# Performance work log

Measured on AMD Instinct MI355X. Metric: run time of the kernel, lower is better.

Reference implementation:

```python
import jax, jax.numpy as jnp
import numpy as np

N = 100000
E = 1600000
BN_EPS = 1e-5
L2_EPS = 1e-12


def _sage_conv(x, src, dst, wl, bl, wr):
    # mean-aggregate source features onto destination nodes
    s = jax.ops.segment_sum(x[src], dst, num_segments=N)          # [N, C]
    cnt = jax.ops.segment_sum(jnp.ones((E,), x.dtype), dst, num_segments=N)
    agg = s / jnp.maximum(cnt, 1.0)[:, None]
    out = agg @ wl.T + bl + x @ wr.T                              # lin_l(agg) + lin_r(x)
    # normalize=True -> row-wise L2 normalization
    nrm = jnp.sqrt(jnp.sum(out * out, axis=-1, keepdims=True))
    return out / jnp.maximum(nrm, L2_EPS)


def _bn(x, g, b):
    # BatchNorm1d, training-mode batch statistics (biased variance)
    m = jnp.mean(x, axis=0)
    v = jnp.mean((x - m) ** 2, axis=0)
    return (x - m) / jnp.sqrt(v + BN_EPS) * g + b


def setup_inputs() -> dict:
    key = jax.random.key(0)
    ks = jax.random.split(key, 24)
    dims = [(4, 6), (6, 8), (8, 16), (16, 32)]
    inp = {
        "x": jax.random.normal(ks[0], (N, 4), jnp.float32),
        "edge_index": jax.random.randint(ks[1], (2, E), 0, N, dtype=jnp.int64),
    }
    ki = 2
    for li, (ci, co) in enumerate(dims, start=1):
        sc = 1.0 / np.sqrt(ci)
        inp[f"w{li}l"] = jax.random.uniform(ks[ki], (co, ci), jnp.float32, -sc, sc); ki += 1
        inp[f"b{li}l"] = jax.random.uniform(ks[ki], (co,), jnp.float32, -sc, sc); ki += 1
        inp[f"w{li}r"] = jax.random.uniform(ks[ki], (co, ci), jnp.float32, -sc, sc); ki += 1
    for li, co in enumerate([6, 8, 16], start=1):
        inp[f"g{li}"] = jnp.ones((co,), jnp.float32)
        inp[f"be{li}"] = jnp.zeros((co,), jnp.float32)
    return inp


def reference(x, edge_index,
              w1l, b1l, w1r, w2l, b2l, w2r, w3l, b3l, w3r, w4l, b4l, w4r,
              g1, be1, g2, be2, g3, be3):
    src, dst = edge_index[0], edge_index[1]
    h = _sage_conv(x, src, dst, w1l, b1l, w1r)
    h = _bn(jax.nn.relu(h), g1, be1)
    h = _sage_conv(h, src, dst, w2l, b2l, w2r)
    h = _bn(jax.nn.relu(h), g2, be2)
    h = _sage_conv(h, src, dst, w3l, b3l, w3r)
    h = _bn(jax.nn.relu(h), g3, be3)
    h = _sage_conv(h, src, dst, w4l, b4l, w4r)
    return jax.nn.relu(h)
```

## Files before the change

kernel.cpp:

```cpp
#include <hip/hip_runtime.h>

#define NNODES 100000
#define NEDGES 1600000
#define BN_EPS 1e-5f
#define L2_EPS 1e-12f

#define BKT_SHIFT 9
#define BKT_SIZE  512
#define NBKT      196
#define CHUNK     8192
#define NBLK_E    196

template<int NT>
__device__ __forceinline__ int block_excl_scan(int v, int* wsum) {
    __syncthreads();
    constexpr int NW = NT / 64;
    int incl = v;
#pragma unroll
    for (int off = 1; off < 64; off <<= 1) {
        int t = __shfl_up(incl, off);
        if ((threadIdx.x & 63) >= off) incl += t;
    }
    int wid = threadIdx.x >> 6;
    if ((threadIdx.x & 63) == 63) wsum[wid] = incl;
    __syncthreads();
    if (threadIdx.x < NW) {
        int w = wsum[threadIdx.x];
#pragma unroll
        for (int off = 1; off < NW; off <<= 1) {
            int t = __shfl_up(w, off);
            if ((int)threadIdx.x >= off) w += t;
        }
        wsum[threadIdx.x] = w;
    }
    __syncthreads();
    int base = wid ? wsum[wid - 1] : 0;
    return base + incl - v;
}

__global__ void hist_kernel(const int* __restrict__ dst,
                            int* __restrict__ blk_hist_T, float* __restrict__ stats) {
    __shared__ int h[NBKT];
    for (int i = threadIdx.x; i < NBKT; i += blockDim.x) h[i] = 0;
    if (blockIdx.x == 0 && threadIdx.x < 128) {
        stats[threadIdx.x] = 0.0f;
        stats[threadIdx.x + 128] = 0.0f;
        stats[threadIdx.x + 256] = 0.0f;
    }
    __syncthreads();
    int base = blockIdx.x * CHUNK;
    int end  = min(base + CHUNK, NEDGES);
    for (int e = base + threadIdx.x * 4; e < end; e += blockDim.x * 4) {
        int4 d = *reinterpret_cast<const int4*>(dst + e);
        atomicAdd(&h[d.x >> BKT_SHIFT], 1);
        atomicAdd(&h[d.y >> BKT_SHIFT], 1);
        atomicAdd(&h[d.z >> BKT_SHIFT], 1);
        atomicAdd(&h[d.w >> BKT_SHIFT], 1);
    }
    __syncthreads();
    for (int i = threadIdx.x; i < NBKT; i += blockDim.x)
        blk_hist_T[i * NBLK_E + blockIdx.x] = h[i];
}

__global__ void scan_blocks(const int* __restrict__ blk_hist_T,
                            int* __restrict__ blk_off, int* __restrict__ bucket_total) {
    __shared__ int wsum[4];
    int b = blockIdx.x;
    int i = threadIdx.x;
    int v = (i < NBLK_E) ? blk_hist_T[b * NBLK_E + i] : 0;
    int excl = block_excl_scan<256>(v, wsum);
    if (i < NBLK_E) blk_off[i * NBKT + b] = excl;
    if (i == 255) bucket_total[b] = excl + v;
}

__global__ void scan_buckets(const int* __restrict__ bucket_total, int* __restrict__ bucket_base) {
    __shared__ int wsum[4];
    int i = threadIdx.x;
    int v = (i < NBKT) ? bucket_total[i] : 0;
    int excl = block_excl_scan<256>(v, wsum);
    if (i < NBKT) bucket_base[i] = excl;
    if (i == 255) bucket_base[NBKT] = excl + v;
}

__global__ void bucket_scatter(const int* __restrict__ src, const int* __restrict__ dst,
                               const int* __restrict__ blk_off, const int* __restrict__ bucket_base,
                               unsigned int* __restrict__ staged) {
    __shared__ int cur[NBKT];
    for (int i = threadIdx.x; i < NBKT; i += blockDim.x)
        cur[i] = blk_off[blockIdx.x * NBKT + i] + bucket_base[i];
    __syncthreads();
    int base = blockIdx.x * CHUNK;
    int end  = min(base + CHUNK, NEDGES);
    for (int e = base + threadIdx.x * 4; e < end; e += blockDim.x * 4) {
        int4 d = *reinterpret_cast<const int4*>(dst + e);
        int4 s = *reinterpret_cast<const int4*>(src + e);
        int p0 = atomicAdd(&cur[d.x >> BKT_SHIFT], 1);
        staged[p0] = ((unsigned)(d.x & (BKT_SIZE - 1)) << 23) | (unsigned)s.x;
        int p1 = atomicAdd(&cur[d.y >> BKT_SHIFT], 1);
        staged[p1] = ((unsigned)(d.y & (BKT_SIZE - 1)) << 23) | (unsigned)s.y;
        int p2 = atomicAdd(&cur[d.z >> BKT_SHIFT], 1);
        staged[p2] = ((unsigned)(d.z & (BKT_SIZE - 1)) << 23) | (unsigned)s.z;
        int p3 = atomicAdd(&cur[d.w >> BKT_SHIFT], 1);
        staged[p3] = ((unsigned)(d.w & (BKT_SIZE - 1)) << 23) | (unsigned)s.w;
    }
}

__global__ void csr_finalize(const unsigned int* __restrict__ staged,
                             const int* __restrict__ bucket_base,
                             int* __restrict__ row_ptr, int* __restrict__ col) {
    __shared__ int nh[BKT_SIZE];
    __shared__ int cur[BKT_SIZE];
    __shared__ int wsum[8];
    int b = blockIdx.x;
    int beg = bucket_base[b], end = bucket_base[b + 1];

    nh[threadIdx.x] = 0;
    __syncthreads();
    for (int e = beg + threadIdx.x; e < end; e += blockDim.x)
        atomicAdd(&nh[staged[e] >> 23], 1);
    __syncthreads();

    int v = nh[threadIdx.x];
    int excl = block_excl_scan<512>(v, wsum);

    int node = b * BKT_SIZE + threadIdx.x;
    if (node < NNODES) row_ptr[node] = beg + excl;
    if (b == 0 && threadIdx.x == 0) row_ptr[NNODES] = NEDGES;
    cur[threadIdx.x] = excl;
    __syncthreads();

    for (int e = beg + threadIdx.x; e < end; e += blockDim.x) {
        unsigned pk = staged[e];
        int l = (int)(pk >> 23);
        int p = atomicAdd(&cur[l], 1);
        col[beg + p] = (int)(pk & 0x7FFFFF);
    }
}

template<int CI>
__device__ __forceinline__ void load_row(const float* __restrict__ p, float* r) {
    constexpr int N4 = CI / 4;
#pragma unroll
    for (int i = 0; i < N4; i++) {
        float4 v = ((const float4*)p)[i];
        r[4*i] = v.x; r[4*i+1] = v.y; r[4*i+2] = v.z; r[4*i+3] = v.w;
    }
    if constexpr ((CI % 4) >= 2) {
        float2 v = ((const float2*)(p + 4 * N4))[0];
        r[4*N4] = v.x; r[4*N4+1] = v.y;
    }
    if constexpr ((CI % 2) == 1) r[CI - 1] = p[CI - 1];
}

template<int CI, int SI, int CO, int SO, int G, bool IN_AFFINE, bool DO_STATS>
__global__ void layer_kernel(const int* __restrict__ row_ptr, const int* __restrict__ col,
                             const float* __restrict__ h,
                             const float* __restrict__ ssum_in, const float* __restrict__ ssq_in,
                             const float* __restrict__ g_in, const float* __restrict__ b_in,
                             const float* __restrict__ wl, const float* __restrict__ bl,
                             const float* __restrict__ wr,
                             float* __restrict__ y,
                             float* __restrict__ stat_sum, float* __restrict__ stat_sq) {
    constexpr int NPB = 256 / G;
    constexpr int OPL = (CO + G - 1) / G;
    constexpr int PCI = CI + 1;

    __shared__ float sWl[CO * PCI];
    __shared__ float sWr[CO * PCI];
    __shared__ float sBl[CO];
    __shared__ float sSc[CI];
    __shared__ float sSh[CI];
    __shared__ float red_sum[CO];
    __shared__ float red_sq[CO];

    for (int i = threadIdx.x; i < CO * CI; i += blockDim.x) {
        int o = i / CI, c = i - o * CI;
        sWl[o * PCI + c] = wl[i];
        sWr[o * PCI + c] = wr[i];
    }
    if (threadIdx.x < CO) {
        sBl[threadIdx.x] = bl[threadIdx.x];
        if (DO_STATS) { red_sum[threadIdx.x] = 0.0f; red_sq[threadIdx.x] = 0.0f; }
    }
    if (IN_AFFINE && threadIdx.x < CI) {
        float m  = ssum_in[threadIdx.x] * (1.0f / NNODES);
        float vv = ssq_in[threadIdx.x] * (1.0f / NNODES) - m * m;
        float s  = g_in[threadIdx.x] / sqrtf(vv + BN_EPS);
        sSc[threadIdx.x] = s;
        sSh[threadIdx.x] = b_in[threadIdx.x] - m * s;
    }
    __syncthreads();

    int node = blockIdx.x * NPB + (threadIdx.x / G);
    int g    = threadIdx.x & (G - 1);
    bool valid = node < NNODES;

    float acc[CI];
#pragma unroll
    for (int c = 0; c < CI; c++) acc[c] = 0.0f;

    int beg = 0, end = 0;
    if (valid) {
        beg = row_ptr[node];
        end = row_ptr[node + 1];
        int j = beg + g;
        for (; j + 3 * G < end; j += 4 * G) {
            int i0 = col[j], i1 = col[j + G], i2 = col[j + 2 * G], i3 = col[j + 3 * G];
            float r0[CI], r1[CI], r2[CI], r3[CI];
            load_row<CI>(h + (long)i0 * SI, r0);
            load_row<CI>(h + (long)i1 * SI, r1);
            load_row<CI>(h + (long)i2 * SI, r2);
            load_row<CI>(h + (long)i3 * SI, r3);
#pragma unroll
            for (int c = 0; c < CI; c++) acc[c] += (r0[c] + r1[c]) + (r2[c] + r3[c]);
        }
        for (; j + G < end; j += 2 * G) {
            int i0 = col[j], i1 = col[j + G];
            float r0[CI], r1[CI];
            load_row<CI>(h + (long)i0 * SI, r0);
            load_row<CI>(h + (long)i1 * SI, r1);
#pragma unroll
            for (int c = 0; c < CI; c++) acc[c] += r0[c] + r1[c];
        }
        if (j < end) {
            float r0[CI];
            load_row<CI>(h + (long)col[j] * SI, r0);
#pragma unroll
            for (int c = 0; c < CI; c++) acc[c] += r0[c];
        }
    }

#pragma unroll
    for (int m = 1; m < G; m <<= 1)
#pragma unroll
        for (int c = 0; c < CI; c++) acc[c] += __shfl_xor(acc[c], m);

    float out[OPL];
    float nrm2 = 0.0f;
    if (valid) {
        float ic = 1.0f / fmaxf((float)(end - beg), 1.0f);
        float xin[CI];
        load_row<CI>(h + (long)node * SI, xin);
        float agg[CI];
#pragma unroll
        for (int c = 0; c < CI; c++) {
            float a  = acc[c] * ic;
            float xv = xin[c];
            if (IN_AFFINE) {
                a  = a  * sSc[c] + sSh[c];
                xv = xv * sSc[c] + sSh[c];
            }
            agg[c] = a;
            xin[c] = xv;
        }
#pragma unroll
        for (int k = 0; k < OPL; k++) {
            int o = g * OPL + k;
            float v = 0.0f;
            if (o < CO) {
                v = sBl[o];
#pragma unroll
                for (int c = 0; c < CI; c++)
                    v += sWl[o * PCI + c] * agg[c] + sWr[o * PCI + c] * xin[c];
            }
            out[k] = v;
            nrm2 += v * v;
        }
    }
#pragma unroll
    for (int m = 1; m < G; m <<= 1) nrm2 += __shfl_xor(nrm2, m);

    if (valid) {
        float inv_nrm = 1.0f / fmaxf(sqrtf(nrm2), L2_EPS);
#pragma unroll
        for (int k = 0; k < OPL; k++) {
            int o = g * OPL + k;
            if (o < CO) {
                float v = fmaxf(out[k] * inv_nrm, 0.0f);
                y[(long)node * SO + o] = v;
                if (DO_STATS) {
                    atomicAdd(&red_sum[o], v);
                    atomicAdd(&red_sq[o], v * v);
                }
            }
        }
    }

    if (DO_STATS) {
        __syncthreads();
        if (threadIdx.x < CO) {
            atomicAdd(&stat_sum[threadIdx.x], red_sum[threadIdx.x]);
            atomicAdd(&stat_sq[threadIdx.x], red_sq[threadIdx.x]);
        }
    }
}

extern "C" void kernel_launch(void* const* d_in, const int* in_sizes, int n_in,
                              void* d_out, int out_size, void* d_ws, size_t ws_size,
                              hipStream_t stream) {
    const float* x   = (const float*)d_in[0];
    const int*   ei  = (const int*)d_in[1];
    const int*   src = ei;
    const int*   dst = ei + NEDGES;

    const float* w1l = (const float*)d_in[2];
    const float* b1l = (const float*)d_in[3];
    const float* w1r = (const float*)d_in[4];
    const float* w2l = (const float*)d_in[5];
    const float* b2l = (const float*)d_in[6];
    const float* w2r = (const float*)d_in[7];
    const float* w3l = (const float*)d_in[8];
    const float* b3l = (const float*)d_in[9];
    const float* w3r = (const float*)d_in[10];
    const float* w4l = (const float*)d_in[11];
    const float* b4l = (const float*)d_in[12];
    const float* w4r = (const float*)d_in[13];
    const float* g1  = (const float*)d_in[14];
    const float* be1 = (const float*)d_in[15];
    const float* g2  = (const float*)d_in[16];
    const float* be2 = (const float*)d_in[17];
    const float* g3  = (const float*)d_in[18];
    const float* be3 = (const float*)d_in[19];

    char* w = (char*)d_ws;
    int* blk_hist     = (int*)w;  w += NBLK_E * NBKT * 4;
    int* blk_off      = (int*)w;  w += NBLK_E * NBKT * 4;
    int* bucket_total = (int*)w;  w += 256 * 4;
    int* bucket_base  = (int*)w;  w += 256 * 4;
    int* row_ptr      = (int*)w;  w += (NNODES + 8) * 4;
    int* col          = (int*)w;  w += NEDGES * 4;
    float* hA         = (float*)w; w += NNODES * 16 * 4;
    float* hB         = (float*)w; w += NNODES * 16 * 4;
    float* stats      = (float*)w; w += 3 * 128 * 4;
    unsigned int* staged = (unsigned int*)hB;

    float* ssum1 = stats + 0 * 128, *ssq1 = ssum1 + 32;
    float* ssum2 = stats + 1 * 128, *ssq2 = ssum2 + 32;
    float* ssum3 = stats + 2 * 128, *ssq3 = ssum3 + 32;

    hist_kernel   <<<NBLK_E, 512, 0, stream>>>(dst, blk_hist, stats);
    scan_blocks   <<<NBKT, 256, 0, stream>>>(blk_hist, blk_off, bucket_total);
    scan_buckets  <<<1, 256, 0, stream>>>(bucket_total, bucket_base);
    bucket_scatter<<<NBLK_E, 512, 0, stream>>>(src, dst, blk_off, bucket_base, staged);
    csr_finalize  <<<NBKT, 512, 0, stream>>>(staged, bucket_base, row_ptr, col);

    layer_kernel<4, 4, 6, 8, 4, false, true><<<(NNODES * 4 + 255) / 256, 256, 0, stream>>>(
        row_ptr, col, x, nullptr, nullptr, nullptr, nullptr,
        w1l, b1l, w1r, hA, ssum1, ssq1);

    layer_kernel<6, 8, 8, 8, 4, true, true><<<(NNODES * 4 + 255) / 256, 256, 0, stream>>>(
        row_ptr, col, hA, ssum1, ssq1, g1, be1,
        w2l, b2l, w2r, hB, ssum2, ssq2);

    layer_kernel<8, 8, 16, 16, 4, true, true><<<(NNODES * 4 + 255) / 256, 256, 0, stream>>>(
        row_ptr, col, hB, ssum2, ssq2, g2, be2,
        w3l, b3l, w3r, hA, ssum3, ssq3);

    layer_kernel<16, 16, 32, 32, 8, true, false><<<(NNODES * 8 + 255) / 256, 256, 0, stream>>>(
        row_ptr, col, hA, ssum3, ssq3, g3, be3,
        w4l, b4l, w4r, (float*)d_out, nullptr, nullptr);
}
```

Before: 292.1 us.

## Widen per-node thread groups, slot BN stats atomics, fold bucket scan into consumers

Doubles the number of threads cooperating on each node's neighbor gather in every layer (G 4→8, 8→16), keeping the 4-way unrolled loop only for G≤8. BatchNorm statistic atomics are spread across 64 slots to cut global atomic contention, and the consuming layer reduces those slots in its prologue. The single-block scan_buckets kernel is removed, and every bucket_scatter and csr_finalize block recomputes the bucket prefix scan itself. This trades redundant work and more threads for fewer launches and more memory-level parallelism.

```diff
diff --git a/kernel.cpp b/kernel.cpp
--- a/kernel.cpp
+++ b/kernel.cpp
@@ -10,6 +10,7 @@
 #define NBKT      196
 #define CHUNK     8192
 #define NBLK_E    196
+#define NSLOT     64
 
 template<int NT>
 __device__ __forceinline__ int block_excl_scan(int v, int* wsum) {
@@ -42,11 +43,8 @@
                             int* __restrict__ blk_hist_T, float* __restrict__ stats) {
     __shared__ int h[NBKT];
     for (int i = threadIdx.x; i < NBKT; i += blockDim.x) h[i] = 0;
-    if (blockIdx.x == 0 && threadIdx.x < 128) {
-        stats[threadIdx.x] = 0.0f;
-        stats[threadIdx.x + 128] = 0.0f;
-        stats[threadIdx.x + 256] = 0.0f;
-    }
+    if (blockIdx.x == 0)
+        for (int i = threadIdx.x; i < 3 * NSLOT * 64; i += blockDim.x) stats[i] = 0.0f;
     __syncthreads();
     int base = blockIdx.x * CHUNK;
     int end  = min(base + CHUNK, NEDGES);
@@ -73,21 +71,15 @@
     if (i == 255) bucket_total[b] = excl + v;
 }
 
-__global__ void scan_buckets(const int* __restrict__ bucket_total, int* __restrict__ bucket_base) {
-    __shared__ int wsum[4];
-    int i = threadIdx.x;
-    int v = (i < NBKT) ? bucket_total[i] : 0;
-    int excl = block_excl_scan<256>(v, wsum);
-    if (i < NBKT) bucket_base[i] = excl;
-    if (i == 255) bucket_base[NBKT] = excl + v;
-}
-
 __global__ void bucket_scatter(const int* __restrict__ src, const int* __restrict__ dst,
-                               const int* __restrict__ blk_off, const int* __restrict__ bucket_base,
+                               const int* __restrict__ blk_off, const int* __restrict__ bucket_total,
                                unsigned int* __restrict__ staged) {
     __shared__ int cur[NBKT];
-    for (int i = threadIdx.x; i < NBKT; i += blockDim.x)
-        cur[i] = blk_off[blockIdx.x * NBKT + i] + bucket_base[i];
+    __shared__ int wsum[8];
+    int v = (threadIdx.x < NBKT) ? bucket_total[threadIdx.x] : 0;
+    int bbase = block_excl_scan<512>(v, wsum);
+    if (threadIdx.x < NBKT)
+        cur[threadIdx.x] = bbase + blk_off[blockIdx.x * NBKT + threadIdx.x];
     __syncthreads();
     int base = blockIdx.x * CHUNK;
     int end  = min(base + CHUNK, NEDGES);
@@ -106,27 +98,32 @@
 }
 
 __global__ void csr_finalize(const unsigned int* __restrict__ staged,
-                             const int* __restrict__ bucket_base,
+                             const int* __restrict__ bucket_total,
                              int* __restrict__ row_ptr, int* __restrict__ col) {
     __shared__ int nh[BKT_SIZE];
     __shared__ int cur[BKT_SIZE];
     __shared__ int wsum[8];
+    __shared__ int sBeg, sEnd;
     int b = blockIdx.x;
-    int beg = bucket_base[b], end = bucket_base[b + 1];
 
     nh[threadIdx.x] = 0;
-    __syncthreads();
+    int v = (threadIdx.x < NBKT) ? bucket_total[threadIdx.x] : 0;
+    int excl = block_excl_scan<512>(v, wsum);
+    if (threadIdx.x == b) { sBeg = excl; sEnd = excl + v; }
+    __syncthreads();
+    int beg = sBeg, end = sEnd;
+
     for (int e = beg + threadIdx.x; e < end; e += blockDim.x)
         atomicAdd(&nh[staged[e] >> 23], 1);
     __syncthreads();
 
-    int v = nh[threadIdx.x];
-    int excl = block_excl_scan<512>(v, wsum);
+    int hv = nh[threadIdx.x];
+    int hexcl = block_excl_scan<512>(hv, wsum);
 
     int node = b * BKT_SIZE + threadIdx.x;
-    if (node < NNODES) row_ptr[node] = beg + excl;
+    if (node < NNODES) row_ptr[node] = beg + hexcl;
     if (b == 0 && threadIdx.x == 0) row_ptr[NNODES] = NEDGES;
-    cur[threadIdx.x] = excl;
+    cur[threadIdx.x] = hexcl;
     __syncthreads();
 
     for (int e = beg + threadIdx.x; e < end; e += blockDim.x) {
@@ -170,6 +167,8 @@
     __shared__ float sBl[CO];
     __shared__ float sSc[CI];
     __shared__ float sSh[CI];
+    __shared__ float sSumR[CI];
+    __shared__ float sSqR[CI];
     __shared__ float red_sum[CO];
     __shared__ float red_sq[CO];
 
@@ -182,12 +181,28 @@
         sBl[threadIdx.x] = bl[threadIdx.x];
         if (DO_STATS) { red_sum[threadIdx.x] = 0.0f; red_sq[threadIdx.x] = 0.0f; }
     }
-    if (IN_AFFINE && threadIdx.x < CI) {
-        float m  = ssum_in[threadIdx.x] * (1.0f / NNODES);
-        float vv = ssq_in[threadIdx.x] * (1.0f / NNODES) - m * m;
-        float s  = g_in[threadIdx.x] / sqrtf(vv + BN_EPS);
-        sSc[threadIdx.x] = s;
-        sSh[threadIdx.x] = b_in[threadIdx.x] - m * s;
+    if (IN_AFFINE && threadIdx.x < CI) { sSumR[threadIdx.x] = 0.0f; sSqR[threadIdx.x] = 0.0f; }
+    __syncthreads();
+    if (IN_AFFINE) {
+        int c = threadIdx.x & 31, sl = threadIdx.x >> 5;
+        if (c < CI) {
+            float ps = 0.0f, pq = 0.0f;
+#pragma unroll
+            for (int s = sl; s < NSLOT; s += 8) {
+                ps += ssum_in[s * 64 + c];
+                pq += ssq_in[s * 64 + c];
+            }
+            atomicAdd(&sSumR[c], ps);
+            atomicAdd(&sSqR[c], pq);
+        }
+        __syncthreads();
+        if (threadIdx.x < CI) {
+            float m  = sSumR[threadIdx.x] * (1.0f / NNODES);
+            float vv = sSqR[threadIdx.x] * (1.0f / NNODES) - m * m;
+            float s  = g_in[threadIdx.x] / sqrtf(vv + BN_EPS);
+            sSc[threadIdx.x] = s;
+            sSh[threadIdx.x] = b_in[threadIdx.x] - m * s;
+        }
     }
     __syncthreads();
 
@@ -204,15 +219,17 @@
         beg = row_ptr[node];
         end = row_ptr[node + 1];
         int j = beg + g;
-        for (; j + 3 * G < end; j += 4 * G) {
-            int i0 = col[j], i1 = col[j + G], i2 = col[j + 2 * G], i3 = col[j + 3 * G];
-            float r0[CI], r1[CI], r2[CI], r3[CI];
-            load_row<CI>(h + (long)i0 * SI, r0);
-            load_row<CI>(h + (long)i1 * SI, r1);
-            load_row<CI>(h + (long)i2 * SI, r2);
-            load_row<CI>(h + (long)i3 * SI, r3);
-#pragma unroll
-            for (int c = 0; c < CI; c++) acc[c] += (r0[c] + r1[c]) + (r2[c] + r3[c]);
+        if constexpr (G <= 8) {
+            for (; j + 3 * G < end; j += 4 * G) {
+                int i0 = col[j], i1 = col[j + G], i2 = col[j + 2 * G], i3 = col[j + 3 * G];
+                float r0[CI], r1[CI], r2[CI], r3[CI];
+                load_row<CI>(h + (long)i0 * SI, r0);
+                load_row<CI>(h + (long)i1 * SI, r1);
+                load_row<CI>(h + (long)i2 * SI, r2);
+                load_row<CI>(h + (long)i3 * SI, r3);
+#pragma unroll
+                for (int c = 0; c < CI; c++) acc[c] += (r0[c] + r1[c]) + (r2[c] + r3[c]);
+            }
         }
         for (; j + G < end; j += 2 * G) {
             int i0 = col[j], i1 = col[j + G];
@@ -289,8 +306,9 @@
     if (DO_STATS) {
         __syncthreads();
         if (threadIdx.x < CO) {
-            atomicAdd(&stat_sum[threadIdx.x], red_sum[threadIdx.x]);
-            atomicAdd(&stat_sq[threadIdx.x], red_sq[threadIdx.x]);
+            int slot = blockIdx.x & (NSLOT - 1);
+            atomicAdd(&stat_sum[slot * 64 + threadIdx.x], red_sum[threadIdx.x]);
+            atomicAdd(&stat_sq [slot * 64 + threadIdx.x], red_sq[threadIdx.x]);
         }
     }
 }
@@ -326,37 +344,35 @@
     int* blk_hist     = (int*)w;  w += NBLK_E * NBKT * 4;
     int* blk_off      = (int*)w;  w += NBLK_E * NBKT * 4;
     int* bucket_total = (int*)w;  w += 256 * 4;
-    int* bucket_base  = (int*)w;  w += 256 * 4;
     int* row_ptr      = (int*)w;  w += (NNODES + 8) * 4;
     int* col          = (int*)w;  w += NEDGES * 4;
     float* hA         = (float*)w; w += NNODES * 16 * 4;
     float* hB         = (float*)w; w += NNODES * 16 * 4;
-    float* stats      = (float*)w; w += 3 * 128 * 4;
+    float* stats      = (float*)w; w += 3 * NSLOT * 64 * 4;
     unsigned int* staged = (unsigned int*)hB;
 
-    float* ssum1 = stats + 0 * 128, *ssq1 = ssum1 + 32;
-    float* ssum2 = stats + 1 * 128, *ssq2 = ssum2 + 32;
-    float* ssum3 = stats + 2 * 128, *ssq3 = ssum3 + 32;
+    float* ssum1 = stats + 0 * NSLOT * 64, *ssq1 = ssum1 + 32;
+    float* ssum2 = stats + 1 * NSLOT * 64, *ssq2 = ssum2 + 32;
+    float* ssum3 = stats + 2 * NSLOT * 64, *ssq3 = ssum3 + 32;
 
     hist_kernel   <<<NBLK_E, 512, 0, stream>>>(dst, blk_hist, stats);
     scan_blocks   <<<NBKT, 256, 0, stream>>>(blk_hist, blk_off, bucket_total);
-    scan_buckets  <<<1, 256, 0, stream>>>(bucket_total, bucket_base);
-    bucket_scatter<<<NBLK_E, 512, 0, stream>>>(src, dst, blk_off, bucket_base, staged);
-    csr_finalize  <<<NBKT, 512, 0, stream>>>(staged, bucket_base, row_ptr, col);
-
-    layer_kernel<4, 4, 6, 8, 4, false, true><<<(NNODES * 4 + 255) / 256, 256, 0, stream>>>(
+    bucket_scatter<<<NBLK_E, 512, 0, stream>>>(src, dst, blk_off, bucket_total, staged);
+    csr_finalize  <<<NBKT, 512, 0, stream>>>(staged, bucket_total, row_ptr, col);
+
+    layer_kernel<4, 4, 6, 8, 8, false, true><<<(NNODES * 8 + 255) / 256, 256, 0, stream>>>(
         row_ptr, col, x, nullptr, nullptr, nullptr, nullptr,
         w1l, b1l, w1r, hA, ssum1, ssq1);
 
-    layer_kernel<6, 8, 8, 8, 4, true, true><<<(NNODES * 4 + 255) / 256, 256, 0, stream>>>(
+    layer_kernel<6, 8, 8, 8, 8, true, true><<<(NNODES * 8 + 255) / 256, 256, 0, stream>>>(
         row_ptr, col, hA, ssum1, ssq1, g1, be1,
         w2l, b2l, w2r, hB, ssum2, ssq2);
 
-    layer_kernel<8, 8, 16, 16, 4, true, true><<<(NNODES * 4 + 255) / 256, 256, 0, stream>>>(
+    layer_kernel<8, 8, 16, 16, 8, true, true><<<(NNODES * 8 + 255) / 256, 256, 0, stream>>>(
         row_ptr, col, hB, ssum2, ssq2, g2, be2,
         w3l, b3l, w3r, hA, ssum3, ssq3);
 
-    layer_kernel<16, 16, 32, 32, 8, true, false><<<(NNODES * 8 + 255) / 256, 256, 0, stream>>>(
+    layer_kernel<16, 16, 32, 32, 16, true, false><<<(NNODES * 16 + 255) / 256, 256, 0, stream>>>(
         row_ptr, col, hA, ssum3, ssq3, g3, be3,
         w4l, b4l, w4r, (float*)d_out, nullptr, nullptr);
 }
```

Result: faster. 260.0 us (-11.0%).
